# Performance work log

Measured on AMD Instinct MI355X. Metric: run time of the kernel, lower is better.

## Reference

```python
import jax, jax.numpy as jnp
import numpy as np

N_NODE = 200000   # item catalog size (n_node)
EMB = 100         # emb_size
NNZ = 1000000     # hypergraph adjacency nonzeros
B = 1024          # batch / cl_size
L = 50            # session length
LAYERS = 2        # HyperConv layers (opt.layer)
TAU = 0.2         # contrastive temperature
K_NEI = 3         # FindNeighbors.neighbor_n


def setup_inputs() -> dict:
    key = jax.random.key(0)
    ks = jax.random.split(key, 16)
    g = 1.414 / np.sqrt(EMB)  # xavier_normal gain=1.414 scale
    inp = {}
    inp["embedding"] = jax.random.normal(ks[0], (N_NODE, EMB), jnp.float32) * 0.1
    inp["adj_val"] = jax.random.uniform(ks[1], (NNZ,), jnp.float32)
    inp["A"] = jax.random.uniform(ks[2], (B, B), jnp.float32) * 0.01
    inp["D"] = jax.random.uniform(ks[3], (B, B), jnp.float32) * 0.01
    inp["z2"] = jax.random.normal(ks[4], (B, EMB), jnp.float32)
    inp["Wcf1"] = jax.random.normal(ks[5], (EMB, EMB), jnp.float32) * g
    inp["bcf1"] = jnp.zeros((EMB,), jnp.float32)
    inp["Wcf2"] = jax.random.normal(ks[6], (EMB, EMB), jnp.float32) * g
    inp["bcf2"] = jnp.zeros((EMB,), jnp.float32)
    inp["Wkg1"] = jax.random.normal(ks[7], (EMB, EMB), jnp.float32) * g
    inp["bkg1"] = jnp.zeros((EMB,), jnp.float32)
    inp["Wkg2"] = jax.random.normal(ks[8], (EMB, EMB), jnp.float32) * g
    inp["bkg2"] = jnp.zeros((EMB,), jnp.float32)
    inp["session_len"] = jnp.full((B, 1), float(L), jnp.float32)
    inp["adj_row"] = jax.random.randint(ks[9], (NNZ,), 0, N_NODE, jnp.int32)
    inp["adj_col"] = jax.random.randint(ks[10], (NNZ,), 0, N_NODE, jnp.int32)
    inp["items"] = jax.random.randint(ks[11], (B, L), 0, N_NODE + 1, jnp.int32)
    return inp


def _proj(z, W1, b1, W2, b2):
    # nn.Linear -> ELU -> nn.Linear (Contrast_2view projector)
    return jax.nn.elu(z @ W1.T + b1) @ W2.T + b2


def reference(embedding, adj_val, A, D, z2,
              Wcf1, bcf1, Wcf2, bcf2, Wkg1, bkg1, Wkg2, bkg2,
              session_len, adj_row, adj_col, items):
    # ---- HyperConv: layered sparse propagation, averaged over layers ----
    h = embedding
    acc = embedding
    for _ in range(LAYERS):
        # torch.sparse.mm(adjacency, h) via gather + segment_sum
        h = jax.ops.segment_sum(adj_val[:, None] * h[adj_col], adj_row,
                                num_segments=N_NODE)
        acc = acc + h
    hyper = acc / (LAYERS + 1)  # [N_NODE, EMB]

    # ---- RelationGAT.forward ----
    emb_pad = jnp.concatenate([jnp.zeros((1, EMB), hyper.dtype), hyper], axis=0)
    seq_h = emb_pad[items]                       # [B, L, EMB]
    rel = jnp.sum(seq_h, axis=1) / session_len   # [B, EMB]
    rel = (D @ A) @ rel                          # session-graph conv
    c = jax.nn.selu(rel)
    l_c = c / jnp.linalg.norm(c, axis=-1, keepdims=True)  # [B, EMB]

    # ---- FindNeighbors (dropout omitted: eval mode) ----
    sess = l_c
    norms = jnp.sqrt(jnp.sum(sess * sess + 1e-6, axis=1, keepdims=True))
    cos = (sess @ sess.T) / (norms @ norms.T)    # [B, B]
    cos = jax.nn.softmax(cos, axis=-1)
    topv, topi = jax.lax.top_k(cos, K_NEI)       # [B, K]
    topv = jax.nn.softmax(topv, axis=-1)
    neighbor = jnp.sum(topv[:, :, None] * sess[topi], axis=1)  # [B, EMB]

    # ---- Contrast_2view ----
    z1p = _proj(sess, Wcf1, bcf1, Wcf2, bcf2)
    z2p = _proj(z2, Wkg1, bkg1, Wkg2, bkg2)
    n1 = jnp.linalg.norm(z1p, axis=-1, keepdims=True)
    n2 = jnp.linalg.norm(z2p, axis=-1, keepdims=True)
    simm = jnp.exp((z1p @ z2p.T) / (n1 @ n2.T) / TAU)
    simm = simm / (jnp.sum(simm, axis=1, keepdims=True) + 1e-8)
    cl_loss = -jnp.mean(jnp.log(jnp.diagonal(simm)))  # pos = eye

    return hyper, l_c, neighbor, cl_loss
```

## Files before the change

### kernel.cpp

```cpp
#include <hip/hip_runtime.h>
#include <hip/hip_bf16.h>

#define N_NODE 200000
#define EMB 100
#define NNZ 1000000
#define BATCH 1024
#define SLEN 50
#define BE (BATCH * EMB)
#define SCAN_BLK 1024
#define PROJ_ROWS 8
#define UNR 8
#define HIST_BLOCKS 977
#define REPACK_BLOCKS 12500

#define OFF_LC    20000000LL
#define OFF_NB    20102400LL
#define OFF_LOSS  20204800LL

typedef __hip_bfloat16 bf16;

__device__ __forceinline__ float b2f(bf16 x) { return __bfloat162float(x); }
__device__ __forceinline__ bf16 f2b(float x) { return __float2bfloat16(x); }

__device__ __forceinline__ float ldf(const void* p, long long i, int f32) {
    return f32 ? ((const float*)p)[i] : b2f(((const bf16*)p)[i]);
}
__device__ __forceinline__ void stf(void* p, long long i, int f32, float v) {
    if (f32) ((float*)p)[i] = v;
    else     ((bf16*)p)[i] = f2b(v);
}

__device__ __forceinline__ float bfb2f(unsigned short s) {
    return __uint_as_float(((unsigned)s) << 16);
}
__device__ __forceinline__ unsigned short f2bfb(float x) {
    bf16 h = f2b(x); unsigned short r; __builtin_memcpy(&r, &h, 2); return r;
}
__device__ __forceinline__ float2 up2(unsigned u) {
    return make_float2(bfb2f((unsigned short)(u & 0xffff)), bfb2f((unsigned short)(u >> 16)));
}
__device__ __forceinline__ unsigned pk2(float a, float b) {
    return (unsigned)f2bfb(a) | ((unsigned)f2bfb(b) << 16);
}
__device__ __forceinline__ float2 ldf2(const void* p, long long pi, int f32) {
    if (f32) return ((const float2*)p)[pi];
    return up2(((const unsigned*)p)[pi]);
}
template<bool F32>
__device__ __forceinline__ float2 ldf2t(const void* p, long long pi) {
    if (F32) return ((const float2*)p)[pi];
    return up2(((const unsigned*)p)[pi]);
}
__device__ __forceinline__ void stf2(void* p, long long pi, int f32, float a, float b) {
    if (f32) ((float2*)p)[pi] = make_float2(a, b);
    else     ((unsigned*)p)[pi] = pk2(a, b);
}

__device__ __forceinline__ float wave_allreduce_sum(float v) {
    for (int m = 32; m > 0; m >>= 1) v += __shfl_xor(v, m, 64);
    return v;
}

__global__ void hist_repack(const int* __restrict__ rows, int* __restrict__ counts,
                            const void* __restrict__ adjval, int* __restrict__ flag,
                            const void* __restrict__ emb, void* __restrict__ embp,
                            int f32h) {
    if (blockIdx.x == 0 && threadIdx.x == 0) {
        int f = 0;
        const bf16* p = (const bf16*)adjval;
        for (int i = 0; i < 64; i++) {
            float x = b2f(p[i]);
            if (!(x >= 0.0f && x <= 1.0f)) f = 1;
        }
        *flag = f;
    }
    if (blockIdx.x < HIST_BLOCKS) {
        int e0 = (blockIdx.x * 256 + threadIdx.x) * 4;
        if (e0 < NNZ) {
            int4 r4 = *(const int4*)&rows[e0];
            atomicAdd(&counts[r4.x], 1);
            atomicAdd(&counts[r4.y], 1);
            atomicAdd(&counts[r4.z], 1);
            atomicAdd(&counts[r4.w], 1);
        }
        return;
    }
    long long idx = (long long)(blockIdx.x - HIST_BLOCKS) * 256 + threadIdx.x;
    if (idx >= (long long)N_NODE * 16) return;
    long long r = idx >> 4;
    int l0 = (int)(idx & 15) * 4;
    #pragma unroll
    for (int j = 0; j < 4; j++) {
        int l = l0 + j;
        float2 v = make_float2(0.f, 0.f);
        if (l < 50) v = ldf2(emb, r * 50 + l, f32h);
        stf2(embp, r * 64 + l, f32h, v.x, v.y);
    }
}

__global__ void scan_base(const int* __restrict__ counts, int* __restrict__ cursor,
                          int2* __restrict__ bc, int* __restrict__ gtot) {
    __shared__ int s[SCAN_BLK];
    __shared__ int basesh;
    int i = blockIdx.x * SCAN_BLK + threadIdx.x;
    int v = (i < N_NODE) ? counts[i] : 0;
    s[threadIdx.x] = v;
    __syncthreads();
    for (int off = 1; off < SCAN_BLK; off <<= 1) {
        int add = (threadIdx.x >= (unsigned)off) ? s[threadIdx.x - off] : 0;
        __syncthreads();
        s[threadIdx.x] += add;
        __syncthreads();
    }
    if (threadIdx.x == SCAN_BLK - 1) basesh = atomicAdd(gtot, s[threadIdx.x]);
    __syncthreads();
    if (i < N_NODE) {
        int ex = s[threadIdx.x] - v + basesh;
        cursor[i] = ex;
        bc[i] = make_int2(ex, v);
    }
}

__global__ void permute_edges(const int* __restrict__ arow, const int* __restrict__ acol,
                              const void* __restrict__ aval, int* __restrict__ cursor,
                              int2* __restrict__ cv, const int* __restrict__ flagp) {
    const int f32 = *flagp;
    int e = blockIdx.x * 256 + threadIdx.x;
    if (blockIdx.x == 0 && threadIdx.x < 8) cv[NNZ + threadIdx.x] = make_int2(0, 0);
    if (e >= NNZ) return;
    int r = arow[e];
    int pos = atomicAdd(&cursor[r], 1);
    float v = ldf(aval, e, f32);
    cv[pos] = make_int2(acol[e], __float_as_int(v));
}

__device__ __forceinline__ void ld_cv8(int2* c, const int2* __restrict__ cv, int k0) {
    #pragma unroll
    for (int j = 0; j < UNR; j++) c[j] = cv[k0 + j];
}

template<bool F32>
__device__ __forceinline__ void spmm1_body(
        const int2* __restrict__ bc, const int2* __restrict__ cv,
        const void* __restrict__ src, int estride, unsigned* __restrict__ h1) {
    int lane = threadIdx.x & 63;
    int r = blockIdx.x * 4 + (threadIdx.x >> 6);
    if (r >= N_NODE) return;
    bool act = lane < 50;
    int pl = (estride == 64) ? lane : (act ? lane : 0);
    int2 b = bc[r];
    int k0 = b.x, k1 = b.x + b.y;
    int2 c[UNR];
    ld_cv8(c, cv, k0);
    int c0x = c[0].x;
    float2 e[UNR];
    #pragma unroll
    for (int j = 0; j < UNR; j++) {
        int cl = (k0 + j < k1) ? c[j].x : c0x;
        e[j] = ldf2t<F32>(src, (long long)cl * estride + pl);
    }
    float a0 = 0.f, a1 = 0.f;
    #pragma unroll
    for (int j = 0; j < UNR; j++) {
        float v = (k0 + j < k1) ? __int_as_float(c[j].y) : 0.f;
        a0 += v * e[j].x; a1 += v * e[j].y;
    }
    for (int k = k0 + UNR; k < k1; k += UNR) {
        int2 ct[UNR];
        #pragma unroll
        for (int j = 0; j < UNR; j++) { int kk = k + j; ct[j] = cv[kk < k1 ? kk : k1 - 1]; }
        float2 et[UNR];
        #pragma unroll
        for (int j = 0; j < UNR; j++)
            et[j] = ldf2t<F32>(src, (long long)ct[j].x * estride + pl);
        #pragma unroll
        for (int j = 0; j < UNR; j++) {
            float v = (k + j < k1) ? __int_as_float(ct[j].y) : 0.f;
            a0 += v * et[j].x; a1 += v * et[j].y;
        }
    }
    h1[(long long)r * 64 + lane] = pk2(a0, a1);
}

__global__ __launch_bounds__(256) void spmm_gather1(
        const int2* __restrict__ bc, const int2* __restrict__ cv,
        const void* __restrict__ src, int estride,
        unsigned* __restrict__ h1, const int* __restrict__ flagp) {
    if (*flagp) spmm1_body<true>(bc, cv, src, estride, h1);
    else        spmm1_body<false>(bc, cv, src, estride, h1);
}

template<bool F32>
__device__ __forceinline__ void spmm2_body(
        const int2* __restrict__ bc, const int2* __restrict__ cv,
        const void* __restrict__ emb,
        const unsigned* __restrict__ h1, void* __restrict__ out) {
    int lane = threadIdx.x & 63;
    int r = blockIdx.x * 4 + (threadIdx.x >> 6);
    if (r >= N_NODE) return;
    bool act = lane < 50;
    int pl = act ? lane : 0;
    int2 b = bc[r];
    int k0 = b.x, k1 = b.x + b.y;
    int2 c[UNR];
    ld_cv8(c, cv, k0);
    int c0x = c[0].x;
    float2 ebv = ldf2t<F32>(emb, (long long)r * 50 + pl);
    float2 h1r = up2(h1[(long long)r * 64 + lane]);
    float2 e[UNR];
    #pragma unroll
    for (int j = 0; j < UNR; j++) {
        int cl = (k0 + j < k1) ? c[j].x : c0x;
        e[j] = up2(h1[(long long)cl * 64 + lane]);
    }
    float a0 = 0.f, a1 = 0.f;
    #pragma unroll
    for (int j = 0; j < UNR; j++) {
        float v = (k0 + j < k1) ? __int_as_float(c[j].y) : 0.f;
        a0 += v * e[j].x; a1 += v * e[j].y;
    }
    for (int k = k0 + UNR; k < k1; k += UNR) {
        int2 ct[UNR];
        #pragma unroll
        for (int j = 0; j < UNR; j++) { int kk = k + j; ct[j] = cv[kk < k1 ? kk : k1 - 1]; }
        float2 et[UNR];
        #pragma unroll
        for (int j = 0; j < UNR; j++)
            et[j] = up2(h1[(long long)ct[j].x * 64 + lane]);
        #pragma unroll
        for (int j = 0; j < UNR; j++) {
            float v = (k + j < k1) ? __int_as_float(ct[j].y) : 0.f;
            a0 += v * et[j].x; a1 += v * et[j].y;
        }
    }
    if (act)
        stf2(out, (long long)r * 50 + lane, F32 ? 1 : 0,
             (ebv.x + h1r.x + a0) * (1.0f / 3.0f), (ebv.y + h1r.y + a1) * (1.0f / 3.0f));
}

__global__ __launch_bounds__(256) void spmm_gather2(
        const int2* __restrict__ bc, const int2* __restrict__ cv,
        const void* __restrict__ emb,
        const unsigned* __restrict__ h1, void* __restrict__ out,
        const int* __restrict__ flagp) {
    if (*flagp) spmm2_body<true>(bc, cv, emb, h1, out);
    else        spmm2_body<false>(bc, cv, emb, h1, out);
}

template<bool F32>
__device__ __forceinline__ void rel_rows_body(
        const void* __restrict__ out, const int* __restrict__ items,
        const void* __restrict__ slen, float* __restrict__ rel) {
    int lane = threadIdx.x & 63;
    int b = blockIdx.x * 4 + (threadIdx.x >> 6);
    if (b >= BATCH || lane >= 50) return;
    float s0 = 0.f, s1 = 0.f;
    #pragma unroll
    for (int l0 = 0; l0 < SLEN; l0 += 10) {
        int it[10];
        #pragma unroll
        for (int j = 0; j < 10; j++) it[j] = items[b * SLEN + l0 + j];
        float2 e[10];
        #pragma unroll
        for (int j = 0; j < 10; j++) {
            int idx = (it[j] > 0) ? it[j] - 1 : 0;
            e[j] = ldf2t<F32>(out, (long long)idx * 50 + lane);
        }
        #pragma unroll
        for (int j = 0; j < 10; j++) {
            float m = (it[j] > 0) ? 1.f : 0.f;
            s0 += m * e[j].x; s1 += m * e[j].y;
        }
    }
    float inv = 1.0f / ldf(slen, b, F32 ? 1 : 0);
    ((float2*)rel)[b * 50 + lane] = make_float2(s0 * inv, s1 * inv);
}

__global__ __launch_bounds__(256) void rel_rows(
        const void* __restrict__ out, const int* __restrict__ items,
        const void* __restrict__ slen, float* __restrict__ rel,
        const int* __restrict__ flagp) {
    if (*flagp) rel_rows_body<true>(out, items, slen, rel);
    else        rel_rows_body<false>(out, items, slen, rel);
}

__device__ __forceinline__ void bmm0_dev(float* smem, const void* __restrict__ M,
                                         const float* __restrict__ X, float* __restrict__ Y,
                                         int f32, int blk) {
    float (*ms)[BATCH] = (float(*)[BATCH])smem;
    int i0 = blk * 4;
    int t = threadIdx.x;
    for (int idx = t; idx < 4 * BATCH; idx += 256) {
        int rr = idx >> 10, j = idx & 1023;
        ms[rr][j] = ldf(M, (long long)(i0 + rr) * BATCH + j, f32);
    }
    __syncthreads();
    int w = t >> 6, lane = t & 63;
    if (lane >= 50) return;
    int i = i0 + w;
    const float2* X2 = (const float2*)X;
    float s0 = 0.f, s1 = 0.f;
    for (int j = 0; j < BATCH; j++) {
        float m = ms[w][j];
        float2 x = X2[j * 50 + lane];
        s0 += m * x.x; s1 += m * x.y;
    }
    ((float2*)Y)[i * 50 + lane] = make_float2(s0, s1);
}

__device__ void proj_dev(float* smem, const void* __restrict__ X, int x_dual,
                         const void* __restrict__ W1, const void* __restrict__ B1,
                         const void* __restrict__ W2, const void* __restrict__ B2,
                         float* __restrict__ Z, float* __restrict__ ZT,
                         float* __restrict__ nrm, int f32, int blk) {
    float* wT = smem;
    float* bsh = smem + 10000;
    float (*hid)[EMB] = (float(*)[EMB])(smem + 10100);
    float (*xr)[EMB]  = (float(*)[EMB])(smem + 10900);
    float (*red2)[2]  = (float(*)[2])(smem + 11100);
    int t = threadIdx.x;
    int sub = t >> 7, u = t & 127;
    int r0 = blk * PROJ_ROWS;
    for (int idx = t; idx < EMB * EMB; idx += 256) {
        int o = idx / EMB, k = idx - o * EMB;
        wT[k * EMB + o] = ldf(W1, idx, f32);
    }
    if (t < EMB) bsh[t] = ldf(B1, t, f32);
    __syncthreads();
    for (int pr = 0; pr < PROJ_ROWS; pr += 2) {
        int row = r0 + pr + sub;
        if (u < EMB)
            xr[sub][u] = x_dual ? ldf(X, (long long)row * EMB + u, f32)
                                : ((const float*)X)[row * EMB + u];
        __syncthreads();
        if (u < EMB) {
            float s = bsh[u];
            for (int k = 0; k < EMB; k++) s += xr[sub][k] * wT[k * EMB + u];
            hid[pr + sub][u] = (s > 0.f) ? s : expm1f(s);
        }
        __syncthreads();
    }
    for (int idx = t; idx < EMB * EMB; idx += 256) {
        int o = idx / EMB, k = idx - o * EMB;
        wT[k * EMB + o] = ldf(W2, idx, f32);
    }
    if (t < EMB) bsh[t] = ldf(B2, t, f32);
    __syncthreads();
    for (int pr = 0; pr < PROJ_ROWS; pr += 2) {
        int row = r0 + pr + sub;
        float sq = 0.f;
        if (u < EMB) {
            float o = bsh[u];
            const float* h = hid[pr + sub];
            for (int k = 0; k < EMB; k++) o += h[k] * wT[k * EMB + u];
            Z[(long long)row * EMB + u] = o;
            if (ZT) ZT[(long long)u * BATCH + row] = o;
            sq = o * o;
        }
        sq = wave_allreduce_sum(sq);
        if ((t & 63) == 0) red2[sub][(t >> 6) & 1] = sq;
        __syncthreads();
        if (u == 0) nrm[row] = sqrtf(red2[sub][0] + red2[sub][1]);
        __syncthreads();
    }
}

__device__ void proj_loss_dev(float* smem, const float* __restrict__ X,
                              const void* __restrict__ W1, const void* __restrict__ B1,
                              const void* __restrict__ W2, const void* __restrict__ B2,
                              const float* __restrict__ z2pT, const float* __restrict__ n2,
                              float* __restrict__ lacc, int* __restrict__ done,
                              void* __restrict__ out, int f32, int blk) {
    float* wT = smem;
    float* bsh = smem + 10000;
    float (*hid)[EMB] = (float(*)[EMB])(smem + 10100);
    float (*xr)[EMB]  = (float(*)[EMB])(smem + 10900);
    float (*red2)[2]  = (float(*)[2])(smem + 11100);
    float (*zsh)[EMB] = (float(*)[EMB])(smem + 11104);
    float* n1sh = smem + 11904;
    float* sd   = smem + 11912;
    float* red  = smem + 11913;
    int t = threadIdx.x;
    int sub = t >> 7, u = t & 127;
    int r0 = blk * PROJ_ROWS;
    for (int idx = t; idx < EMB * EMB; idx += 256) {
        int o = idx / EMB, k = idx - o * EMB;
        wT[k * EMB + o] = ldf(W1, idx, f32);
    }
    if (t < EMB) bsh[t] = ldf(B1, t, f32);
    __syncthreads();
    for (int pr = 0; pr < PROJ_ROWS; pr += 2) {
        int row = r0 + pr + sub;
        if (u < EMB) xr[sub][u] = X[(long long)row * EMB + u];
        __syncthreads();
        if (u < EMB) {
            float s = bsh[u];
            for (int k = 0; k < EMB; k++) s += xr[sub][k] * wT[k * EMB + u];
            hid[pr + sub][u] = (s > 0.f) ? s : expm1f(s);
        }
        __syncthreads();
    }
    for (int idx = t; idx < EMB * EMB; idx += 256) {
        int o = idx / EMB, k = idx - o * EMB;
        wT[k * EMB + o] = ldf(W2, idx, f32);
    }
    if (t < EMB) bsh[t] = ldf(B2, t, f32);
    __syncthreads();
    for (int pr = 0; pr < PROJ_ROWS; pr += 2) {
        float sq = 0.f;
        float o = 0.f;
        if (u < EMB) {
            o = bsh[u];
            const float* h = hid[pr + sub];
            for (int k = 0; k < EMB; k++) o += h[k] * wT[k * EMB + u];
            sq = o * o;
        }
        __syncthreads();
        if (u < EMB) zsh[pr + sub][u] = o;
        sq = wave_allreduce_sum(sq);
        if ((t & 63) == 0) red2[sub][(t >> 6) & 1] = sq;
        __syncthreads();
        if (u == 0) n1sh[pr + sub] = sqrtf(red2[sub][0] + red2[sub][1]);
        __syncthreads();
    }
    float blockloss = 0.f;
    for (int rr = 0; rr < PROJ_ROWS; rr++) {
        int i = r0 + rr;
        float ni = n1sh[rr];
        float d0 = 0.f, d1 = 0.f, d2 = 0.f, d3 = 0.f;
        for (int k = 0; k < EMB; k++) {
            float zv = zsh[rr][k];
            const float* row = z2pT + k * BATCH;
            d0 += zv * row[t];
            d1 += zv * row[t + 256];
            d2 += zv * row[t + 512];
            d3 += zv * row[t + 768];
        }
        float e0 = expf(d0 / (ni * n2[t]) * 5.0f);
        float e1 = expf(d1 / (ni * n2[t + 256]) * 5.0f);
        float e2 = expf(d2 / (ni * n2[t + 512]) * 5.0f);
        float e3 = expf(d3 / (ni * n2[t + 768]) * 5.0f);
        if (t == (i & 255)) {
            int m = i >> 8;
            sd[0] = (m == 0) ? e0 : (m == 1) ? e1 : (m == 2) ? e2 : e3;
        }
        float local = e0 + e1 + e2 + e3;
        float w = wave_allreduce_sum(local);
        if ((t & 63) == 0) red[t >> 6] = w;
        __syncthreads();
        if (t == 0) {
            float S = red[0] + red[1] + red[2] + red[3];
            blockloss += -logf(sd[0] / (S + 1e-8f));
        }
        __syncthreads();
    }
    if (t == 0) {
        atomicAdd(lacc, blockloss * (1.0f / BATCH));
        __threadfence();
        int old = atomicAdd(done, 1);
        if (old == BATCH / PROJ_ROWS - 1) {
            float v = atomicAdd(lacc, 0.0f);
            stf(out, OFF_LOSS, f32, v);
        }
    }
}

__global__ __launch_bounds__(256) void bmm1_projz2(
        const void* __restrict__ A, const float* __restrict__ relv, float* __restrict__ t1,
        const void* __restrict__ z2,
        const void* __restrict__ W1, const void* __restrict__ B1,
        const void* __restrict__ W2, const void* __restrict__ B2,
        float* __restrict__ z2p, float* __restrict__ z2pT, float* __restrict__ n2,
        const int* __restrict__ flagp) {
    __shared__ float smem[11104];
    const int f32 = *flagp;
    if (blockIdx.x < 256) bmm0_dev(smem, A, relv, t1, f32, blockIdx.x);
    else proj_dev(smem, z2, 1, W1, B1, W2, B2, z2p, z2pT, n2, f32, blockIdx.x - 256);
}

__global__ __launch_bounds__(256) void bmm2_selu(const void* __restrict__ M,
                                                 const float* __restrict__ X,
                                                 float* __restrict__ sess,
                                                 float* __restrict__ sessT,
                                                 float* __restrict__ ns,
                                                 void* __restrict__ out,
                                                 float* __restrict__ lacc,
                                                 int* __restrict__ done,
                                                 const int* __restrict__ flagp) {
    __shared__ float ms[4][BATCH];
    const int f32 = *flagp;
    if (blockIdx.x == 0 && threadIdx.x == 0) { *lacc = 0.f; *done = 0; }
    int i0 = blockIdx.x * 4;
    int t = threadIdx.x;
    for (int idx = t; idx < 4 * BATCH; idx += 256) {
        int rr = idx >> 10, j = idx & 1023;
        ms[rr][j] = ldf(M, (long long)(i0 + rr) * BATCH + j, f32);
    }
    __syncthreads();
    int w = t >> 6, lane = t & 63;
    bool act = lane < 50;
    int i = i0 + w;
    float s0 = 0.f, s1 = 0.f;
    if (act) {
        const float2* X2 = (const float2*)X;
        for (int j = 0; j < BATCH; j++) {
            float m = ms[w][j];
            float2 x = X2[j * 50 + lane];
            s0 += m * x.x; s1 += m * x.y;
        }
    }
    const float sc = 1.0507009873554804934193349852946f;
    const float al = 1.6732632423543772848170429916717f;
    float c0 = (s0 > 0.f) ? sc * s0 : sc * (al * expm1f(s0));
    float c1 = (s1 > 0.f) ? sc * s1 : sc * (al * expm1f(s1));
    if (!act) { c0 = 0.f; c1 = 0.f; }
    float nrm = sqrtf(wave_allreduce_sum(c0 * c0 + c1 * c1));
    float l0 = c0 / nrm, l1 = c1 / nrm;
    float nterm = act ? (l0 * l0 + l1 * l1 + 2e-6f) : 0.f;
    float n2sum = wave_allreduce_sum(nterm);
    if (act) {
        ((float2*)sess)[i * 50 + lane] = make_float2(l0, l1);
        sessT[(2 * lane) * BATCH + i] = l0;
        sessT[(2 * lane + 1) * BATCH + i] = l1;
        stf2(out, OFF_LC / 2 + (long long)i * 50 + lane, f32, l0, l1);
    }
    if (lane == 0) ns[i] = sqrtf(n2sum);
}

__device__ void neighbor_dev(float* smem, const float* __restrict__ sess,
                             const float* __restrict__ sessT, const float* __restrict__ ns,
                             void* __restrict__ out, int f32, int i) {
    float* si  = smem;
    float* red = smem + 100;
    float* wrv = smem + 104;
    int*   wri = (int*)(smem + 108);
    float* chv = smem + 112;
    int*   chi = (int*)(smem + 115);
    float* stv = smem + 118;
    int t = threadIdx.x;
    if (t < EMB) si[t] = sess[i * EMB + t];
    __syncthreads();
    float ni = ns[i];
    float d0 = 0.f, d1 = 0.f, d2 = 0.f, d3 = 0.f;
    for (int k = 0; k < EMB; k++) {
        float sv = si[k];
        const float* row = sessT + k * BATCH;
        d0 += sv * row[t];
        d1 += sv * row[t + 256];
        d2 += sv * row[t + 512];
        d3 += sv * row[t + 768];
    }
    float pv0 = expf(d0 / (ni * ns[t]));
    float pv1 = expf(d1 / (ni * ns[t + 256]));
    float pv2 = expf(d2 / (ni * ns[t + 512]));
    float pv3 = expf(d3 / (ni * ns[t + 768]));
    float local = pv0 + pv1 + pv2 + pv3;
    float w = wave_allreduce_sum(local);
    if ((t & 63) == 0) red[t >> 6] = w;
    __syncthreads();
    float S = red[0] + red[1] + red[2] + red[3];

    int c0 = -1, c1 = -1, c2 = -1;
    float pv[4] = {pv0, pv1, pv2, pv3};
    for (int r = 0; r < 3; r++) {
        float bv = -1e30f; int bi = 0x7fffffff;
        #pragma unroll
        for (int m = 0; m < 4; m++) {
            int j = t + (m << 8);
            if (j == c0 || j == c1 || j == c2) continue;
            float v = pv[m];
            if (v > bv || (v == bv && j < bi)) { bv = v; bi = j; }
        }
        #pragma unroll
        for (int off = 1; off < 64; off <<= 1) {
            float ov = __shfl_xor(bv, off);
            int oi = __shfl_xor(bi, off);
            if (ov > bv || (ov == bv && oi < bi)) { bv = ov; bi = oi; }
        }
        if ((t & 63) == 0) { wrv[t >> 6] = bv; wri[t >> 6] = bi; }
        __syncthreads();
        if (t == 0) {
            float fv = wrv[0]; int fi = wri[0];
            for (int wq = 1; wq < 4; wq++) {
                if (wrv[wq] > fv || (wrv[wq] == fv && wri[wq] < fi)) { fv = wrv[wq]; fi = wri[wq]; }
            }
            chv[r] = fv; chi[r] = fi;
        }
        __syncthreads();
        if (r == 0) c0 = chi[0];
        else if (r == 1) c1 = chi[1];
        else c2 = chi[2];
    }
    if (t == 0) {
        float e0 = expf(chv[0] / S), e1 = expf(chv[1] / S), e2 = expf(chv[2] / S);
        float es = e0 + e1 + e2;
        stv[0] = e0 / es; stv[1] = e1 / es; stv[2] = e2 / es;
    }
    __syncthreads();
    if (t < EMB) {
        float o = stv[0] * sess[chi[0] * EMB + t]
                + stv[1] * sess[chi[1] * EMB + t]
                + stv[2] * sess[chi[2] * EMB + t];
        stf(out, OFF_NB + i * EMB + t, f32, o);
    }
}

__global__ __launch_bounds__(256) void neighbor_projz1_loss(
        const float* __restrict__ sess, const float* __restrict__ sessT,
        const float* __restrict__ ns, void* __restrict__ out,
        const void* __restrict__ W1, const void* __restrict__ B1,
        const void* __restrict__ W2, const void* __restrict__ B2,
        const float* __restrict__ z2pT, const float* __restrict__ n2,
        float* __restrict__ lacc, int* __restrict__ done,
        const int* __restrict__ flagp) {
    __shared__ float smem[11920];
    const int f32 = *flagp;
    if (blockIdx.x < BATCH) neighbor_dev(smem, sess, sessT, ns, out, f32, blockIdx.x);
    else proj_loss_dev(smem, sess, W1, B1, W2, B2, z2pT, n2, lacc, done, out, f32,
                       blockIdx.x - BATCH);
}

extern "C" void kernel_launch(void* const* d_in, const int* in_sizes, int n_in,
                              void* d_out, int out_size, void* d_ws, size_t ws_size,
                              hipStream_t stream) {
    const void* emb  = d_in[0];
    const void* aval = d_in[1];
    const void* Amat = d_in[2];
    const void* Dmat = d_in[3];
    const void* z2   = d_in[4];
    const void* Wcf1 = d_in[5];
    const void* bcf1 = d_in[6];
    const void* Wcf2 = d_in[7];
    const void* bcf2 = d_in[8];
    const void* Wkg1 = d_in[9];
    const void* bkg1 = d_in[10];
    const void* Wkg2 = d_in[11];
    const void* bkg2 = d_in[12];
    const void* slen = d_in[13];
    const int* arow  = (const int*)d_in[14];
    const int* acol  = (const int*)d_in[15];
    const int* items = (const int*)d_in[16];

    long long esz = in_sizes ? (long long)in_sizes[0] : 0;
    int f32_host = (esz == (long long)N_NODE * EMB * 4) ? 1 : 0;
    int known_dtype = (esz == (long long)N_NODE * EMB * 2) || f32_host;

    int* flag      = (int*)d_ws;
    int* gtot      = (int*)d_ws + 4;
    int* counts    = (int*)((char*)d_ws + 256);
    int* cursor    = counts;
    int2* bc       = (int2*)(counts + N_NODE);
    int2* cv       = bc + N_NODE;
    unsigned* h1buf = (unsigned*)(cv + NNZ + 8);
    char* tailbase = (char*)(h1buf + (long long)N_NODE * 64);
    void* emb_pad  = (void*)tailbase;
    long long embpad_bytes = (long long)N_NODE * 64 * (f32_host ? 8 : 4);
    float* fsmall  = (float*)tailbase;
    float* rel   = fsmall;
    float* t1    = rel  + BE;
    float* sess  = t1   + BE;
    float* sessT = sess + BE;
    float* z1p   = sessT + BE;
    float* z2p   = z1p  + BE;
    float* z2pT  = z2p  + BE;
    float* ns    = z2pT + BE;
    float* n1    = ns + BATCH;
    float* n2    = n1 + BATCH;
    float* lacc  = n2 + BATCH;
    int*   done  = (int*)(lacc + 1);
    long long fsmall_bytes = ((char*)(done + 16)) - (char*)tailbase;
    long long base_off = tailbase - (char*)d_ws;
    long long need_pad = base_off + (embpad_bytes > fsmall_bytes ? embpad_bytes : fsmall_bytes);
    int use_pad = known_dtype && ((long long)ws_size >= need_pad);
    int estride = use_pad ? 64 : 50;

    const int nscan = (N_NODE + SCAN_BLK - 1) / SCAN_BLK;
    const int repack_blocks = use_pad ? REPACK_BLOCKS : 0;

    hipMemsetAsync(d_ws, 0, 256 + (size_t)N_NODE * sizeof(int), stream);
    hist_repack<<<HIST_BLOCKS + repack_blocks, 256, 0, stream>>>(
        arow, counts, aval, flag, emb, emb_pad, f32_host);
    scan_base<<<nscan, SCAN_BLK, 0, stream>>>(counts, cursor, bc, gtot);
    permute_edges<<<(NNZ + 255) / 256, 256, 0, stream>>>(arow, acol, aval, cursor,
                                                         cv, flag);

    if (use_pad) {
        spmm_gather1<<<(N_NODE + 3) / 4, 256, 0, stream>>>(bc, cv, emb_pad, estride,
                                                           h1buf, flag);
    } else {
        spmm_gather1<<<(N_NODE + 3) / 4, 256, 0, stream>>>(bc, cv, emb, estride,
                                                           h1buf, flag);
    }
    spmm_gather2<<<(N_NODE + 3) / 4, 256, 0, stream>>>(bc, cv, emb, h1buf,
                                                       d_out, flag);

    rel_rows<<<(BATCH + 3) / 4, 256, 0, stream>>>(d_out, items, slen, rel, flag);
    bmm1_projz2<<<384, 256, 0, stream>>>(Amat, rel, t1,
                                         z2, Wkg1, bkg1, Wkg2, bkg2,
                                         z2p, z2pT, n2, flag);
    bmm2_selu<<<BATCH / 4, 256, 0, stream>>>(Dmat, t1, sess, sessT, ns, d_out,
                                             lacc, done, flag);

    neighbor_projz1_loss<<<BATCH + BATCH / PROJ_ROWS, 256, 0, stream>>>(
        sess, sessT, ns, d_out, Wcf1, bcf1, Wcf2, bcf2, z2pT, n2, lacc, done, flag);
}
```

Baseline: 663.5 us.

## Merge CSR build and downstream stages into persistent kernels with grid barriers

Folds histogram, repack, scan and edge permutation into one persistent kernel of 1024 blocks, separated by software grid barriers built on atomics. The four downstream launches (rel_rows, bmm1/projz2, bmm2_selu, neighbor/proj/loss) become a second persistent kernel of 768 blocks that loops over work items with barriers between phases. The goal is to remove kernel launch gaps and tail effects. In exchange, co-residency of all blocks must hold or the barriers deadlock, and some phases run with fewer blocks than before. The barrier counters sit in the workspace region cleared by the existing memset.

```diff
diff --git a/kernel.cpp b/kernel.cpp
--- a/kernel.cpp
+++ b/kernel.cpp
@@ -7,11 +7,12 @@
 #define BATCH 1024
 #define SLEN 50
 #define BE (BATCH * EMB)
-#define SCAN_BLK 1024
 #define PROJ_ROWS 8
 #define UNR 8
-#define HIST_BLOCKS 977
-#define REPACK_BLOCKS 12500
+#define CSR_BLOCKS 1024
+#define CSR_THREADS (CSR_BLOCKS * 256)
+#define SCAN_CHUNKS 196
+#define DS_BLOCKS 768
 
 #define OFF_LC    20000000LL
 #define OFF_NB    20102400LL
@@ -61,77 +62,95 @@
     return v;
 }
 
-__global__ void hist_repack(const int* __restrict__ rows, int* __restrict__ counts,
-                            const void* __restrict__ adjval, int* __restrict__ flag,
-                            const void* __restrict__ emb, void* __restrict__ embp,
-                            int f32h) {
-    if (blockIdx.x == 0 && threadIdx.x == 0) {
+__device__ __forceinline__ void devbar(int* slot, int nb) {
+    __syncthreads();
+    if (threadIdx.x == 0) {
+        __hip_atomic_fetch_add(slot, 1, __ATOMIC_ACQ_REL, __HIP_MEMORY_SCOPE_AGENT);
+        while (__hip_atomic_load(slot, __ATOMIC_ACQUIRE, __HIP_MEMORY_SCOPE_AGENT) < nb)
+            __builtin_amdgcn_s_sleep(2);
+    }
+    __syncthreads();
+}
+
+__global__ __launch_bounds__(256) void csr_build(
+        const int* __restrict__ arow, const int* __restrict__ acol,
+        const void* __restrict__ aval,
+        int* __restrict__ counts,
+        int2* __restrict__ bc, int2* __restrict__ cv,
+        int* __restrict__ flag, int* __restrict__ gtot, int* __restrict__ bar,
+        const void* __restrict__ emb, void* __restrict__ embp,
+        int f32h, int use_pad) {
+    __shared__ int ss[256];
+    __shared__ int basesh;
+    int t = threadIdx.x, blk = blockIdx.x;
+    int tid = blk * 256 + t;
+
+    if (tid == 0) {
         int f = 0;
-        const bf16* p = (const bf16*)adjval;
+        const bf16* p = (const bf16*)aval;
         for (int i = 0; i < 64; i++) {
             float x = b2f(p[i]);
             if (!(x >= 0.0f && x <= 1.0f)) f = 1;
         }
         *flag = f;
     }
-    if (blockIdx.x < HIST_BLOCKS) {
-        int e0 = (blockIdx.x * 256 + threadIdx.x) * 4;
-        if (e0 < NNZ) {
-            int4 r4 = *(const int4*)&rows[e0];
-            atomicAdd(&counts[r4.x], 1);
-            atomicAdd(&counts[r4.y], 1);
-            atomicAdd(&counts[r4.z], 1);
-            atomicAdd(&counts[r4.w], 1);
-        }
-        return;
-    }
-    long long idx = (long long)(blockIdx.x - HIST_BLOCKS) * 256 + threadIdx.x;
-    if (idx >= (long long)N_NODE * 16) return;
-    long long r = idx >> 4;
-    int l0 = (int)(idx & 15) * 4;
-    #pragma unroll
-    for (int j = 0; j < 4; j++) {
-        int l = l0 + j;
-        float2 v = make_float2(0.f, 0.f);
-        if (l < 50) v = ldf2(emb, r * 50 + l, f32h);
-        stf2(embp, r * 64 + l, f32h, v.x, v.y);
-    }
-}
-
-__global__ void scan_base(const int* __restrict__ counts, int* __restrict__ cursor,
-                          int2* __restrict__ bc, int* __restrict__ gtot) {
-    __shared__ int s[SCAN_BLK];
-    __shared__ int basesh;
-    int i = blockIdx.x * SCAN_BLK + threadIdx.x;
-    int v = (i < N_NODE) ? counts[i] : 0;
-    s[threadIdx.x] = v;
-    __syncthreads();
-    for (int off = 1; off < SCAN_BLK; off <<= 1) {
-        int add = (threadIdx.x >= (unsigned)off) ? s[threadIdx.x - off] : 0;
-        __syncthreads();
-        s[threadIdx.x] += add;
-        __syncthreads();
-    }
-    if (threadIdx.x == SCAN_BLK - 1) basesh = atomicAdd(gtot, s[threadIdx.x]);
-    __syncthreads();
-    if (i < N_NODE) {
-        int ex = s[threadIdx.x] - v + basesh;
-        cursor[i] = ex;
-        bc[i] = make_int2(ex, v);
-    }
-}
-
-__global__ void permute_edges(const int* __restrict__ arow, const int* __restrict__ acol,
-                              const void* __restrict__ aval, int* __restrict__ cursor,
-                              int2* __restrict__ cv, const int* __restrict__ flagp) {
-    const int f32 = *flagp;
-    int e = blockIdx.x * 256 + threadIdx.x;
-    if (blockIdx.x == 0 && threadIdx.x < 8) cv[NNZ + threadIdx.x] = make_int2(0, 0);
-    if (e >= NNZ) return;
-    int r = arow[e];
-    int pos = atomicAdd(&cursor[r], 1);
-    float v = ldf(aval, e, f32);
-    cv[pos] = make_int2(acol[e], __float_as_int(v));
+    int e0 = tid * 4;
+    if (e0 < NNZ) {
+        int4 r4 = *(const int4*)&arow[e0];
+        atomicAdd(&counts[r4.x], 1);
+        atomicAdd(&counts[r4.y], 1);
+        atomicAdd(&counts[r4.z], 1);
+        atomicAdd(&counts[r4.w], 1);
+    }
+    if (use_pad) {
+        for (long long idx = tid; idx < (long long)N_NODE * 16; idx += CSR_THREADS) {
+            long long r = idx >> 4;
+            int l0 = (int)(idx & 15) * 4;
+            #pragma unroll
+            for (int j = 0; j < 4; j++) {
+                int l = l0 + j;
+                float2 v = make_float2(0.f, 0.f);
+                if (l < 50) v = ldf2(emb, r * 50 + l, f32h);
+                stf2(embp, r * 64 + l, f32h, v.x, v.y);
+            }
+        }
+    }
+    devbar(&bar[0], CSR_BLOCKS);
+
+    if (blk < SCAN_CHUNKS) {
+        int i0 = blk * 1024 + t * 4;
+        int v0 = 0, v1 = 0, v2 = 0, v3 = 0;
+        if (i0 + 0 < N_NODE) v0 = counts[i0 + 0];
+        if (i0 + 1 < N_NODE) v1 = counts[i0 + 1];
+        if (i0 + 2 < N_NODE) v2 = counts[i0 + 2];
+        if (i0 + 3 < N_NODE) v3 = counts[i0 + 3];
+        int ts = v0 + v1 + v2 + v3;
+        ss[t] = ts;
+        __syncthreads();
+        for (int off = 1; off < 256; off <<= 1) {
+            int add = (t >= off) ? ss[t - off] : 0;
+            __syncthreads();
+            ss[t] += add;
+            __syncthreads();
+        }
+        if (t == 255) basesh = atomicAdd(gtot, ss[255]);
+        __syncthreads();
+        int ex = basesh + ss[t] - ts;
+        if (i0 + 0 < N_NODE) { counts[i0+0] = ex; bc[i0+0] = make_int2(ex, v0); ex += v0; }
+        if (i0 + 1 < N_NODE) { counts[i0+1] = ex; bc[i0+1] = make_int2(ex, v1); ex += v1; }
+        if (i0 + 2 < N_NODE) { counts[i0+2] = ex; bc[i0+2] = make_int2(ex, v2); ex += v2; }
+        if (i0 + 3 < N_NODE) { counts[i0+3] = ex; bc[i0+3] = make_int2(ex, v3); }
+    }
+    devbar(&bar[1], CSR_BLOCKS);
+
+    if (tid < 8) cv[NNZ + tid] = make_int2(0, 0);
+    const int f32 = *flag;
+    for (int e = tid; e < NNZ; e += CSR_THREADS) {
+        int r = arow[e];
+        int pos = atomicAdd(&counts[r], 1);
+        float v = ldf(aval, e, f32);
+        cv[pos] = make_int2(acol[e], __float_as_int(v));
+    }
 }
 
 __device__ __forceinline__ void ld_cv8(int2* c, const int2* __restrict__ cv, int k0) {
@@ -247,46 +266,38 @@
     else        spmm2_body<false>(bc, cv, emb, h1, out);
 }
 
-template<bool F32>
-__device__ __forceinline__ void rel_rows_body(
-        const void* __restrict__ out, const int* __restrict__ items,
-        const void* __restrict__ slen, float* __restrict__ rel) {
+__device__ void rel_rows_dev(const void* __restrict__ out, const int* __restrict__ items,
+                             const void* __restrict__ slen, float* __restrict__ rel,
+                             int f32, int blk) {
     int lane = threadIdx.x & 63;
-    int b = blockIdx.x * 4 + (threadIdx.x >> 6);
-    if (b >= BATCH || lane >= 50) return;
-    float s0 = 0.f, s1 = 0.f;
-    #pragma unroll
-    for (int l0 = 0; l0 < SLEN; l0 += 10) {
-        int it[10];
-        #pragma unroll
-        for (int j = 0; j < 10; j++) it[j] = items[b * SLEN + l0 + j];
-        float2 e[10];
-        #pragma unroll
-        for (int j = 0; j < 10; j++) {
-            int idx = (it[j] > 0) ? it[j] - 1 : 0;
-            e[j] = ldf2t<F32>(out, (long long)idx * 50 + lane);
-        }
-        #pragma unroll
-        for (int j = 0; j < 10; j++) {
-            float m = (it[j] > 0) ? 1.f : 0.f;
-            s0 += m * e[j].x; s1 += m * e[j].y;
-        }
-    }
-    float inv = 1.0f / ldf(slen, b, F32 ? 1 : 0);
-    ((float2*)rel)[b * 50 + lane] = make_float2(s0 * inv, s1 * inv);
-}
-
-__global__ __launch_bounds__(256) void rel_rows(
-        const void* __restrict__ out, const int* __restrict__ items,
-        const void* __restrict__ slen, float* __restrict__ rel,
-        const int* __restrict__ flagp) {
-    if (*flagp) rel_rows_body<true>(out, items, slen, rel);
-    else        rel_rows_body<false>(out, items, slen, rel);
-}
-
-__device__ __forceinline__ void bmm0_dev(float* smem, const void* __restrict__ M,
-                                         const float* __restrict__ X, float* __restrict__ Y,
-                                         int f32, int blk) {
+    int b = blk * 4 + (threadIdx.x >> 6);
+    if (lane < 50) {
+        float s0 = 0.f, s1 = 0.f;
+        #pragma unroll
+        for (int l0 = 0; l0 < SLEN; l0 += 10) {
+            int it[10];
+            #pragma unroll
+            for (int j = 0; j < 10; j++) it[j] = items[b * SLEN + l0 + j];
+            float2 e[10];
+            #pragma unroll
+            for (int j = 0; j < 10; j++) {
+                int idx = (it[j] > 0) ? it[j] - 1 : 0;
+                e[j] = ldf2(out, (long long)idx * 50 + lane, f32);
+            }
+            #pragma unroll
+            for (int j = 0; j < 10; j++) {
+                float m = (it[j] > 0) ? 1.f : 0.f;
+                s0 += m * e[j].x; s1 += m * e[j].y;
+            }
+        }
+        float inv = 1.0f / ldf(slen, b, f32);
+        ((float2*)rel)[b * 50 + lane] = make_float2(s0 * inv, s1 * inv);
+    }
+}
+
+__device__ void bmm0_dev(float* smem, const void* __restrict__ M,
+                         const float* __restrict__ X, float* __restrict__ Y,
+                         int f32, int blk) {
     float (*ms)[BATCH] = (float(*)[BATCH])smem;
     int i0 = blk * 4;
     int t = threadIdx.x;
@@ -296,16 +307,17 @@
     }
     __syncthreads();
     int w = t >> 6, lane = t & 63;
-    if (lane >= 50) return;
-    int i = i0 + w;
-    const float2* X2 = (const float2*)X;
-    float s0 = 0.f, s1 = 0.f;
-    for (int j = 0; j < BATCH; j++) {
-        float m = ms[w][j];
-        float2 x = X2[j * 50 + lane];
-        s0 += m * x.x; s1 += m * x.y;
-    }
-    ((float2*)Y)[i * 50 + lane] = make_float2(s0, s1);
+    if (lane < 50) {
+        int i = i0 + w;
+        const float2* X2 = (const float2*)X;
+        float s0 = 0.f, s1 = 0.f;
+        for (int j = 0; j < BATCH; j++) {
+            float m = ms[w][j];
+            float2 x = X2[j * 50 + lane];
+            s0 += m * x.x; s1 += m * x.y;
+        }
+        ((float2*)Y)[i * 50 + lane] = make_float2(s0, s1);
+    }
 }
 
 __device__ void proj_dev(float* smem, const void* __restrict__ X, int x_dual,
@@ -465,32 +477,13 @@
     }
 }
 
-__global__ __launch_bounds__(256) void bmm1_projz2(
-        const void* __restrict__ A, const float* __restrict__ relv, float* __restrict__ t1,
-        const void* __restrict__ z2,
-        const void* __restrict__ W1, const void* __restrict__ B1,
-        const void* __restrict__ W2, const void* __restrict__ B2,
-        float* __restrict__ z2p, float* __restrict__ z2pT, float* __restrict__ n2,
-        const int* __restrict__ flagp) {
-    __shared__ float smem[11104];
-    const int f32 = *flagp;
-    if (blockIdx.x < 256) bmm0_dev(smem, A, relv, t1, f32, blockIdx.x);
-    else proj_dev(smem, z2, 1, W1, B1, W2, B2, z2p, z2pT, n2, f32, blockIdx.x - 256);
-}
-
-__global__ __launch_bounds__(256) void bmm2_selu(const void* __restrict__ M,
-                                                 const float* __restrict__ X,
-                                                 float* __restrict__ sess,
-                                                 float* __restrict__ sessT,
-                                                 float* __restrict__ ns,
-                                                 void* __restrict__ out,
-                                                 float* __restrict__ lacc,
-                                                 int* __restrict__ done,
-                                                 const int* __restrict__ flagp) {
-    __shared__ float ms[4][BATCH];
-    const int f32 = *flagp;
-    if (blockIdx.x == 0 && threadIdx.x == 0) { *lacc = 0.f; *done = 0; }
-    int i0 = blockIdx.x * 4;
+__device__ void bmm2_selu_dev(float* smem, const void* __restrict__ M,
+                              const float* __restrict__ X,
+                              float* __restrict__ sess, float* __restrict__ sessT,
+                              float* __restrict__ ns, void* __restrict__ out,
+                              int f32, int blk) {
+    float (*ms)[BATCH] = (float(*)[BATCH])smem;
+    int i0 = blk * 4;
     int t = threadIdx.x;
     for (int idx = t; idx < 4 * BATCH; idx += 256) {
         int rr = idx >> 10, j = idx & 1023;
@@ -605,19 +598,45 @@
     }
 }
 
-__global__ __launch_bounds__(256) void neighbor_projz1_loss(
-        const float* __restrict__ sess, const float* __restrict__ sessT,
-        const float* __restrict__ ns, void* __restrict__ out,
-        const void* __restrict__ W1, const void* __restrict__ B1,
-        const void* __restrict__ W2, const void* __restrict__ B2,
-        const float* __restrict__ z2pT, const float* __restrict__ n2,
-        float* __restrict__ lacc, int* __restrict__ done,
+__global__ __launch_bounds__(256, 3) void downstream(
+        void* __restrict__ out, const int* __restrict__ items,
+        const void* __restrict__ slen, float* __restrict__ rel,
+        const void* __restrict__ Amat, float* __restrict__ t1,
+        const void* __restrict__ z2,
+        const void* __restrict__ Wkg1, const void* __restrict__ bkg1,
+        const void* __restrict__ Wkg2, const void* __restrict__ bkg2,
+        float* __restrict__ z2p, float* __restrict__ z2pT, float* __restrict__ n2,
+        const void* __restrict__ Dmat,
+        float* __restrict__ sess, float* __restrict__ sessT, float* __restrict__ ns,
+        const void* __restrict__ Wcf1, const void* __restrict__ bcf1,
+        const void* __restrict__ Wcf2, const void* __restrict__ bcf2,
+        float* __restrict__ lacc, int* __restrict__ done2, int* __restrict__ bar,
         const int* __restrict__ flagp) {
     __shared__ float smem[11920];
     const int f32 = *flagp;
-    if (blockIdx.x < BATCH) neighbor_dev(smem, sess, sessT, ns, out, f32, blockIdx.x);
-    else proj_loss_dev(smem, sess, W1, B1, W2, B2, z2pT, n2, lacc, done, out, f32,
-                       blockIdx.x - BATCH);
+    int blk = blockIdx.x;
+
+    for (int w = blk; w < 256; w += DS_BLOCKS)
+        rel_rows_dev(out, items, slen, rel, f32, w);
+    devbar(&bar[4], DS_BLOCKS);
+
+    for (int w = blk; w < 384; w += DS_BLOCKS) {
+        if (w < 256) bmm0_dev(smem, Amat, rel, t1, f32, w);
+        else proj_dev(smem, z2, 1, Wkg1, bkg1, Wkg2, bkg2, z2p, z2pT, n2, f32, w - 256);
+    }
+    devbar(&bar[5], DS_BLOCKS);
+
+    if (blk == 0 && threadIdx.x == 0) { *lacc = 0.f; *done2 = 0; }
+    for (int w = blk; w < 256; w += DS_BLOCKS)
+        bmm2_selu_dev(smem, Dmat, t1, sess, sessT, ns, out, f32, w);
+    devbar(&bar[6], DS_BLOCKS);
+
+    for (int w = blk; w < 1152; w += DS_BLOCKS) {
+        __syncthreads();
+        if (w < 1024) neighbor_dev(smem, sess, sessT, ns, out, f32, w);
+        else proj_loss_dev(smem, sess, Wcf1, bcf1, Wcf2, bcf2, z2pT, n2,
+                           lacc, done2, out, f32, w - 1024);
+    }
 }
 
 extern "C" void kernel_launch(void* const* d_in, const int* in_sizes, int n_in,
@@ -646,9 +665,9 @@
     int known_dtype = (esz == (long long)N_NODE * EMB * 2) || f32_host;
 
     int* flag      = (int*)d_ws;
-    int* gtot      = (int*)d_ws + 4;
+    int* gtot      = (int*)((char*)d_ws + 16);
+    int* bar       = (int*)((char*)d_ws + 32);
     int* counts    = (int*)((char*)d_ws + 256);
-    int* cursor    = counts;
     int2* bc       = (int2*)(counts + N_NODE);
     int2* cv       = bc + N_NODE;
     unsigned* h1buf = (unsigned*)(cv + NNZ + 8);
@@ -667,22 +686,17 @@
     float* n1    = ns + BATCH;
     float* n2    = n1 + BATCH;
     float* lacc  = n2 + BATCH;
-    int*   done  = (int*)(lacc + 1);
-    long long fsmall_bytes = ((char*)(done + 16)) - (char*)tailbase;
+    int*   done2 = (int*)(lacc + 1);
+    long long fsmall_bytes = ((char*)(done2 + 16)) - (char*)tailbase;
     long long base_off = tailbase - (char*)d_ws;
     long long need_pad = base_off + (embpad_bytes > fsmall_bytes ? embpad_bytes : fsmall_bytes);
     int use_pad = known_dtype && ((long long)ws_size >= need_pad);
     int estride = use_pad ? 64 : 50;
 
-    const int nscan = (N_NODE + SCAN_BLK - 1) / SCAN_BLK;
-    const int repack_blocks = use_pad ? REPACK_BLOCKS : 0;
-
     hipMemsetAsync(d_ws, 0, 256 + (size_t)N_NODE * sizeof(int), stream);
-    hist_repack<<<HIST_BLOCKS + repack_blocks, 256, 0, stream>>>(
-        arow, counts, aval, flag, emb, emb_pad, f32_host);
-    scan_base<<<nscan, SCAN_BLK, 0, stream>>>(counts, cursor, bc, gtot);
-    permute_edges<<<(NNZ + 255) / 256, 256, 0, stream>>>(arow, acol, aval, cursor,
-                                                         cv, flag);
+    csr_build<<<CSR_BLOCKS, 256, 0, stream>>>(arow, acol, aval, counts, bc, cv,
+                                              flag, gtot, bar, emb, emb_pad,
+                                              f32_host, use_pad);
 
     if (use_pad) {
         spmm_gather1<<<(N_NODE + 3) / 4, 256, 0, stream>>>(bc, cv, emb_pad, estride,
@@ -694,13 +708,9 @@
     spmm_gather2<<<(N_NODE + 3) / 4, 256, 0, stream>>>(bc, cv, emb, h1buf,
                                                        d_out, flag);
 
-    rel_rows<<<(BATCH + 3) / 4, 256, 0, stream>>>(d_out, items, slen, rel, flag);
-    bmm1_projz2<<<384, 256, 0, stream>>>(Amat, rel, t1,
-                                         z2, Wkg1, bkg1, Wkg2, bkg2,
-                                         z2p, z2pT, n2, flag);
-    bmm2_selu<<<BATCH / 4, 256, 0, stream>>>(Dmat, t1, sess, sessT, ns, d_out,
-                                             lacc, done, flag);
-
-    neighbor_projz1_loss<<<BATCH + BATCH / PROJ_ROWS, 256, 0, stream>>>(
-        sess, sessT, ns, d_out, Wcf1, bcf1, Wcf2, bcf2, z2pT, n2, lacc, done, flag);
-}
+    downstream<<<DS_BLOCKS, 256, 0, stream>>>(
+        d_out, items, slen, rel, Amat, t1,
+        z2, Wkg1, bkg1, Wkg2, bkg2, z2p, z2pT, n2,
+        Dmat, sess, sessT, ns,
+        Wcf1, bcf1, Wcf2, bcf2, lacc, done2, bar, flag);
+}
```

Result: slower. 2.161 ms (+225.7%).
